# Performance work log

Measured on AMD Instinct MI355X. Metric: run time of the kernel, lower is better.

## Reference

```python
import jax, jax.numpy as jnp
import numpy as np

F_DIM = 64; HID = 256; P_ETA = 32; NBINS = 16; MULT = 3 * NBINS - 1
NLAYERS = 8; NBLOCKS = 2; TAIL = 10.0
MIN_BW = 1e-8; MIN_BH = 1e-8; MIN_D = 1e-8
THETA_DIM = F_DIM + 1
N_BATCH = 8192; M_DATA = 256


def _masks():
    in_deg = np.arange(1, F_DIM + 1)
    hid_deg = np.arange(HID) % (F_DIM - 1) + 1
    out_deg = np.repeat(in_deg, MULT)  # output index f*MULT+m has degree f+1
    m_in = (hid_deg[:, None] >= in_deg[None, :]).astype(np.float32)
    m_hh = (hid_deg[:, None] >= hid_deg[None, :]).astype(np.float32)
    m_out = (out_deg[:, None] > hid_deg[None, :]).astype(np.float32)
    return jnp.asarray(m_in), jnp.asarray(m_hh), jnp.asarray(m_out)


def _rqs_forward(x, uw, uh, ud):
    # unconstrained rational-quadratic spline with linear tails (nflows math)
    const = float(np.log(np.exp(1.0 - MIN_D) - 1.0))
    inside = (x >= -TAIL) & (x <= TAIL)
    ud = jnp.pad(ud, ((0, 0), (0, 0), (1, 1)), constant_values=const)  # [N,F,NBINS+1]
    w = jax.nn.softmax(uw, -1)
    w = MIN_BW + (1.0 - MIN_BW * NBINS) * w
    cw = jnp.concatenate([jnp.zeros_like(w[..., :1]), jnp.cumsum(w, -1)], -1)
    cw = 2.0 * TAIL * cw - TAIL
    cw = cw.at[..., 0].set(-TAIL).at[..., -1].set(TAIL)
    w = jnp.diff(cw, axis=-1)
    h = jax.nn.softmax(uh, -1)
    h = MIN_BH + (1.0 - MIN_BH * NBINS) * h
    ch = jnp.concatenate([jnp.zeros_like(h[..., :1]), jnp.cumsum(h, -1)], -1)
    ch = 2.0 * TAIL * ch - TAIL
    ch = ch.at[..., 0].set(-TAIL).at[..., -1].set(TAIL)
    h = jnp.diff(ch, axis=-1)
    d = MIN_D + jax.nn.softplus(ud)
    xs = jnp.clip(x, -TAIL, TAIL)
    idx = jnp.clip(jnp.sum((xs[..., None] >= cw).astype(jnp.int32), -1) - 1, 0, NBINS - 1)
    g = lambda a, i: jnp.take_along_axis(a, i[..., None], -1)[..., 0]
    icw, ich = g(cw, idx), g(ch, idx)
    iw, ih = g(w, idx), g(h, idx)
    delta = ih / iw
    d0, d1 = g(d, idx), g(d, idx + 1)
    t = (xs - icw) / iw
    tt = t * (1.0 - t)
    denom = delta + (d0 + d1 - 2.0 * delta) * tt
    y = ich + ih * (delta * t * t + d0 * tt) / denom
    dnum = delta * delta * (d1 * t * t + 2.0 * delta * tt + d0 * (1.0 - t) * (1.0 - t))
    ld = jnp.log(dnum) - 2.0 * jnp.log(denom)
    return jnp.where(inside, y, x), jnp.where(inside, ld, 0.0)


def _flow_transform(z, eta, W_in, b_in, W_ctx, b_ctx, W_blk, b_blk, W_out, b_out):
    m_in, m_hh, m_out = _masks()
    sqrt_h = jnp.sqrt(jnp.asarray(HID, z.dtype))

    def layer(carry, p):
        x, ld = carry
        Wi, bi, Wc, bc, Wb, bb, Wo, bo = p
        x = jnp.flip(x, axis=1)  # ReversePermutation (logdet 0)
        h = x @ (Wi * m_in).T + bi + eta @ Wc.T + bc  # MADE initial + context
        for k in range(NBLOCKS):  # masked pre-activation residual blocks
            t = jax.nn.relu(h)
            t = t @ (Wb[k, 0] * m_hh).T + bb[k, 0]
            t = jax.nn.relu(t)
            t = t @ (Wb[k, 1] * m_hh).T + bb[k, 1]
            h = h + t
        out = (h @ (Wo * m_out).T + bo).reshape(x.shape[0], F_DIM, MULT)
        uw = out[..., :NBINS] / sqrt_h
        uh = out[..., NBINS:2 * NBINS] / sqrt_h
        ud = out[..., 2 * NBINS:]
        x, l = _rqs_forward(x, uw, uh, ud)
        return (x, ld + l.sum(-1)), None

    init = (z, jnp.zeros(z.shape[0], z.dtype))
    (x, ld), _ = jax.lax.scan(layer, init, (W_in, b_in, W_ctx, b_ctx, W_blk, b_blk, W_out, b_out))
    return x, ld


def _stick_breaking(x):
    log_v = -jax.nn.softplus(-x)
    log_1v = -jax.nn.softplus(x)
    prefix = jnp.concatenate([jnp.zeros_like(x[:, :1]), jnp.cumsum(log_1v[:, :-1], 1)], 1)
    log_theta = jnp.concatenate([log_v + prefix, log_1v.sum(1, keepdims=True)], 1)
    wts = jnp.arange(F_DIM, 0, -1, dtype=x.dtype)
    log_det = log_v.sum(1) + (wts * log_1v).sum(1)
    return jnp.exp(log_theta), log_det


def setup_inputs() -> dict:
    key = jax.random.key(0)
    ks = jax.random.split(key, 8)
    s = 0.05
    return {
        'z': jax.random.normal(ks[0], (N_BATCH, F_DIM), jnp.float32),
        'eta_batch': jax.random.normal(ks[1], (N_BATCH, P_ETA), jnp.float32),
        'data_D2': jax.random.normal(ks[2], (M_DATA, THETA_DIM), jnp.float32),
        'W_in': s * jax.random.normal(ks[3], (NLAYERS, HID, F_DIM), jnp.float32),
        'b_in': jnp.zeros((NLAYERS, HID), jnp.float32),
        'W_ctx': s * jax.random.normal(ks[4], (NLAYERS, HID, P_ETA), jnp.float32),
        'b_ctx': jnp.zeros((NLAYERS, HID), jnp.float32),
        'W_blk': s * jax.random.normal(ks[5], (NLAYERS, NBLOCKS, 2, HID, HID), jnp.float32),
        'b_blk': jnp.zeros((NLAYERS, NBLOCKS, 2, HID), jnp.float32),
        'W_out': s * jax.random.normal(ks[6], (NLAYERS, F_DIM * MULT, HID), jnp.float32),
        'b_out': jnp.zeros((NLAYERS, F_DIM * MULT), jnp.float32),
    }


def reference(z, eta_batch, data_D2, W_in, b_in, W_ctx, b_ctx, W_blk, b_blk, W_out, b_out):
    x, flow_ld = _flow_transform(z, eta_batch, W_in, b_in, W_ctx, b_ctx, W_blk, b_blk, W_out, b_out)
    theta, sb_ld = _stick_breaking(x)
    total_ld = flow_ld + sb_ld
    log_qz = -0.5 * jnp.sum(z * z, -1) - 0.5 * F_DIM * jnp.log(2.0 * jnp.pi).astype(z.dtype)
    log_q = log_qz - total_ld
    # prior: Dirichlet(alpha=2) unnormalized: sum log(theta)
    log_p = jnp.sum(jnp.log(jnp.clip(theta, 1e-10, None)), -1)
    # likelihood: mean over data rows of isotropic Gaussian centered at theta
    d_sq = jnp.mean(jnp.sum(data_D2 * data_D2, -1))
    d_mean = jnp.mean(data_D2, 0)
    log_lik = -0.5 * (d_sq - 2.0 * theta @ d_mean + jnp.sum(theta * theta, -1))
    return jnp.mean(log_q - (log_p + log_lik))
```

## Files before the change

### kernel.cpp

```cpp
#include <hip/hip_runtime.h>
#include <hip/hip_fp8.h>
#include <math.h>

typedef float f32x4 __attribute__((ext_vector_type(4)));
typedef unsigned short u16;
typedef unsigned char u8;

typedef const __attribute__((address_space(1))) unsigned int ga_u32;
typedef __attribute__((address_space(3))) unsigned int ls_u32;

__device__ __forceinline__ void gl16(const void* g, void* l) {
    __builtin_amdgcn_global_load_lds((ga_u32*)g, (ls_u32*)l, 16, 0, 0);
}

__device__ __forceinline__ u16 f2bf(float f) {
    union { float f; unsigned u; } v; v.f = f;
    return (u16)((v.u + 0x7FFFu + ((v.u >> 16) & 1u)) >> 16);
}
__device__ __forceinline__ float bf2f(u16 h) {
    union { unsigned u; float f; } v; v.u = ((unsigned)h) << 16;
    return v.f;
}
__device__ __forceinline__ u8 f2q(float f) {
    __hip_fp8_e4m3 t(f);
    return (u8)t.__x;
}
__device__ __forceinline__ long ld8(const u8* p) { return *(const long*)p; }

__device__ __forceinline__ float splusf(float x) {
    return fmaxf(x, 0.f) + __logf(1.f + __expf(-fabsf(x)));
}
__device__ __forceinline__ int invperm(int k) {
    int m, q;
    if (k < 20) { m = k / 5; q = k - 5 * m; }
    else        { m = (k - 4) >> 2; q = (k - 4) & 3; }
    return m + 63 * q;
}

#define MID_ACT_P 272
#define WSCALE 64.f
#define WINV (1.f / 64.f)

__global__ __launch_bounds__(256) void setup_w(
    const float* __restrict__ Win, const float* __restrict__ bin,
    const float* __restrict__ Wctx, const float* __restrict__ bctx,
    const float* __restrict__ Wblk, const float* __restrict__ Wout,
    const float* __restrict__ bout, const float* __restrict__ eta,
    u8* __restrict__ W1, float* __restrict__ B1, u8* __restrict__ WB,
    u8* __restrict__ WO, float* __restrict__ BO, u8* __restrict__ AXE)
{
    const long N1 = 8L * 8 * 8 * 64 * 8;
    const long N2 = 8L * 256;
    const long N3 = 8L * 4 * 8 * 16 * 64 * 8;
    const long N4 = 8L * 32 * 8 * 6 * 64 * 8;
    const long N5 = 8L * 3072;
    const long N6 = 8192L * 32;
    const long tot = N1 + N2 + N3 + N4 + N5 + N6;
    for (long i = (long)blockIdx.x * blockDim.x + threadIdx.x; i < tot;
         i += (long)gridDim.x * blockDim.x) {
        long t = i;
        if (t < N1) {
            int off = (int)(t & 7), lane = (int)((t >> 3) & 63);
            int frag = (int)((t >> 9) & 7), wv = (int)((t >> 12) & 7);
            long l = t >> 15;
            int ks = frag >> 1, f = frag & 1;
            int prow = wv * 32 + f * 16 + (lane & 15);
            int row = invperm(prow);
            int c = ks * 32 + ((lane >> 4) << 3) + off;
            float v = 0.f;
            if (c < 64)      v = Win[(l * 256 + row) * 64 + c] * (((row % 63) >= c) ? 1.f : 0.f);
            else if (c < 96) v = Wctx[(l * 256 + row) * 32 + (c - 64)];
            W1[t] = f2q(v * WSCALE);
        } else if ((t -= N1) < N2) {
            long l = t >> 8; int k = (int)(t & 255);
            int c = invperm(k);
            B1[t] = bin[l * 256 + c] + bctx[l * 256 + c];
        } else if ((t -= N2) < N3) {
            int off = (int)(t & 7), lane = (int)((t >> 3) & 63);
            int frag = (int)((t >> 9) & 15), wv = (int)((t >> 13) & 7);
            int bi = (int)((t >> 16) & 3);
            long l = t >> 18;
            int prow = wv * 32 + (frag & 1) * 16 + (lane & 15);
            int pc   = ((frag >> 1) << 5) + ((lane >> 4) << 3) + off;
            int row = invperm(prow), c = invperm(pc);
            float v = Wblk[(((size_t)l * 4 + bi) * 256 + row) * 256 + c] *
                      (((row % 63) >= (c % 63)) ? 1.f : 0.f);
            WB[t] = f2q(v * WSCALE);
        } else if ((t -= N3) < N4) {
            long l = t / 786432; int rem = (int)(t % 786432);
            int y = rem / 24576, r2 = rem % 24576;
            int ks = r2 / 3072, r3 = r2 % 3072;
            int frag = r3 / 512, r4 = r3 % 512;
            int lane = r4 / 8, off = r4 % 8;
            int op = y * 96 + frag * 16 + (lane & 15);
            int pj = ks * 32 + ((lane >> 4) << 3) + off;
            int j = invperm(pj);
            int fd = op / 48, mm = op % 48;
            float v = 0.f;
            if (mm < 47 && fd > (j % 63))
                v = Wout[((size_t)l * 3008 + fd * 47 + mm) * 256 + j];
            WO[t] = f2q(v * WSCALE);
        } else if ((t -= N4) < N5) {
            long l = t / 3072; int op = (int)(t % 3072);
            int fd = op / 48, mm = op % 48;
            BO[t] = (mm < 47) ? bout[l * 3008 + (long)fd * 47 + mm] : 0.f;
        } else {
            t -= N5;
            long b = t / 32; int p = (int)(t % 32);
            AXE[b * 96 + 64 + p] = f2q(eta[t]);
        }
    }
}

__global__ __launch_bounds__(256) void perm_bias(
    const float* __restrict__ bblk, float* __restrict__ BBp)
{
    int t = blockIdx.x * 256 + threadIdx.x;
    int k = t & 255;
    BBp[t] = bblk[(t & ~255) | invperm(k)];
}

__global__ __launch_bounds__(128) void dstat(const float* __restrict__ D,
                                             float* __restrict__ DM)
{
    int j = threadIdx.x;
    float s = 0.f, q = 0.f;
    if (j < 65) {
        for (int m = 0; m < 256; ++m) {
            float v = D[m * 65 + j];
            s += v; q += v * v;
        }
        DM[j] = s * (1.f / 256.f);
    }
    __shared__ float red[128];
    red[j] = q; __syncthreads();
    for (int st = 64; st > 0; st >>= 1) {
        if (j < st) red[j] += red[j + st];
        __syncthreads();
    }
    if (j == 0) DM[65] = red[0] * (1.f / 256.f);
}

__global__ __launch_bounds__(256) void prep0(
    const float* __restrict__ z, float* __restrict__ XF, u8* __restrict__ AXE)
{
    size_t gt = (size_t)blockIdx.x * 256 + threadIdx.x;
    size_t b = gt >> 6; int f = (int)(gt & 63);
    float v = z[b * 64 + (63 - f)];
    XF[gt] = v;
    AXE[b * 96 + f] = f2q(v);
}

template<int NF>
__device__ __forceinline__ void mid_stage_reg(
    const u8* __restrict__ gW, const u8* __restrict__ act,
    int lane, int fr, int kg, f32x4 (&T)[2])
{
    long wf[NF];
#pragma unroll
    for (int j = 0; j < NF; ++j)
        wf[j] = ld8(gW + (j * 64 + lane) * 8);
#pragma unroll
    for (int ks = 0; ks < NF / 2; ++ks) {
        long af = ld8(&act[fr * MID_ACT_P + ks * 32 + kg * 8]);
        T[0] = __builtin_amdgcn_mfma_f32_16x16x32_fp8_fp8(wf[ks * 2 + 0], af, T[0], 0, 0, 0);
        T[1] = __builtin_amdgcn_mfma_f32_16x16x32_fp8_fp8(wf[ks * 2 + 1], af, T[1], 0, 0, 0);
    }
}

__global__ __launch_bounds__(512) void fused_mid(
    const u8* __restrict__ AXE, const u8* __restrict__ W1l,
    const float* __restrict__ B1l, const u8* __restrict__ WBl,
    const float* __restrict__ bbl, u8* __restrict__ HB)
{
    __shared__ u8 act[16 * MID_ACT_P];
    const int tid = threadIdx.x;
    const int lane = tid & 63;
    const int wv = tid >> 6;
    const int fr = lane & 15, kg = lane >> 4;
    const int b0 = blockIdx.x * 16;
    const int ch0 = wv * 32;

    if (tid < 96) {
        int row = tid / 6, part = tid - row * 6;
        *(int4*)&act[row * MID_ACT_P + part * 16] =
            *(const int4*)&AXE[(size_t)(b0 + row) * 96 + part * 16];
    }

    f32x4 H[2], T[2];

    auto zeroT = [&]() {
        T[0] = (f32x4){0.f, 0.f, 0.f, 0.f};
        T[1] = (f32x4){0.f, 0.f, 0.f, 0.f};
    };
    auto epi = [&](const float* bias, int mode) {
#pragma unroll
        for (int m = 0; m < 2; ++m) {
            const int cb = ch0 + m * 16 + kg * 4;
            const float4 bs = *(const float4*)&bias[cb];
            f32x4 v = T[m];
            v[0] = v[0] * WINV + bs.x; v[1] = v[1] * WINV + bs.y;
            v[2] = v[2] * WINV + bs.z; v[3] = v[3] * WINV + bs.w;
            if (mode == 0) H[m] = v;
            if (mode == 2 || mode == 3) {
                H[m][0] += v[0]; H[m][1] += v[1];
                H[m][2] += v[2]; H[m][3] += v[3];
                v = H[m];
            }
            unsigned pk;
            if (mode != 3) {
                pk = (unsigned)f2q(fmaxf(v[0], 0.f))
                   | ((unsigned)f2q(fmaxf(v[1], 0.f)) << 8)
                   | ((unsigned)f2q(fmaxf(v[2], 0.f)) << 16)
                   | ((unsigned)f2q(fmaxf(v[3], 0.f)) << 24);
                *(unsigned*)&act[fr * MID_ACT_P + cb] = pk;
            } else {
                pk = (unsigned)f2q(v[0]) | ((unsigned)f2q(v[1]) << 8)
                   | ((unsigned)f2q(v[2]) << 16) | ((unsigned)f2q(v[3]) << 24);
                const int b = b0 + fr;
                const size_t idx =
                    (((((size_t)(b >> 7) * 8 + (cb >> 5)) * 8 + ((b >> 4) & 7)) * 64)
                     + (((cb >> 3) & 3) * 16 + (b & 15))) * 8 + (cb & 7);
                *(unsigned*)&HB[idx] = pk;
            }
        }
    };

    zeroT();
    __syncthreads();
    mid_stage_reg<6>(W1l + wv * 4096, act, lane, fr, kg, T);
    __syncthreads();
    epi(B1l, 0);
    zeroT();
    __syncthreads();
    mid_stage_reg<16>(WBl + 0 * 65536 + wv * 8192, act, lane, fr, kg, T);
    __syncthreads();
    epi(bbl, 1);
    zeroT();
    __syncthreads();
    mid_stage_reg<16>(WBl + 1 * 65536 + wv * 8192, act, lane, fr, kg, T);
    __syncthreads();
    epi(bbl + 256, 2);
    zeroT();
    __syncthreads();
    mid_stage_reg<16>(WBl + 2 * 65536 + wv * 8192, act, lane, fr, kg, T);
    __syncthreads();
    epi(bbl + 2 * 256, 1);
    zeroT();
    __syncthreads();
    mid_stage_reg<16>(WBl + 3 * 65536 + wv * 8192, act, lane, fr, kg, T);
    __syncthreads();
    epi(bbl + 3 * 256, 3);
}

__global__ __launch_bounds__(256) void gemm_out_spline(
    const u8* __restrict__ A, const u8* __restrict__ Wo,
    const float* __restrict__ bo, const float* __restrict__ XF,
    float* __restrict__ Xn, float* __restrict__ XFnext, u8* __restrict__ AXE,
    float* __restrict__ LDP, int first)
{
    __shared__ u16 SM16[13312];
    u8* SM8 = (u8*)SM16;
    const int tid = threadIdx.x;
    const int lane = tid & 63, wv = tid >> 6;
    const int wm = wv >> 1, wn = wv & 1;
    const int fr = lane & 15, kg = lane >> 4;
    const int by = 31 - (int)blockIdx.y;
    const int m0 = blockIdx.x * 128, n0 = by * 96;
    const int nk = (by + 4) >> 2;

    u8* Ab = SM8;
    u8* Bb = SM8 + 8192;

    const u8* gA = A  + (size_t)blockIdx.x * 16384;
    const u8* gB = Wo + (size_t)by * 24576;

    f32x4 acc[4][3];
#pragma unroll
    for (int m = 0; m < 4; ++m)
#pragma unroll
        for (int n = 0; n < 3; ++n) acc[m][n] = (f32x4){0.f, 0.f, 0.f, 0.f};

    gl16(gA + tid * 16, Ab + tid * 16);
    if (tid < 192) gl16(gB + tid * 16, Bb + tid * 16);

    for (int ks = 0; ks < nk; ++ks) {
        __syncthreads();
        if (ks + 1 < nk) {
            const u8* sa = gA + (ks + 1) * 4096;
            const u8* sb = gB + (ks + 1) * 3072;
            u8* na = Ab + ((ks + 1) & 1) * 4096;
            u8* nb = Bb + ((ks + 1) & 1) * 3072;
            gl16(sa + tid * 16, na + tid * 16);
            if (tid < 192) gl16(sb + tid * 16, nb + tid * 16);
        }
        const u8* cA = Ab + (ks & 1) * 4096;
        const u8* cB = Bb + (ks & 1) * 3072;
        long af[4], bf[3];
#pragma unroll
        for (int m = 0; m < 4; ++m)
            af[m] = ld8(&cA[(wm * 4 + m) * 512 + lane * 8]);
#pragma unroll
        for (int n = 0; n < 3; ++n)
            bf[n] = ld8(&cB[(wn * 3 + n) * 512 + lane * 8]);
#pragma unroll
        for (int m = 0; m < 4; ++m)
#pragma unroll
            for (int n = 0; n < 3; ++n)
                acc[m][n] = __builtin_amdgcn_mfma_f32_16x16x32_fp8_fp8(bf[n], af[m], acc[m][n], 0, 0, 0);
    }
    __syncthreads();

#pragma unroll
    for (int m = 0; m < 4; ++m) {
        const int row = wm * 64 + m * 16 + fr;
#pragma unroll
        for (int n = 0; n < 3; ++n) {
            const int c0 = wn * 48 + n * 16 + kg * 4;
            const float4 bs = *(const float4*)&bo[n0 + c0];
            short4 q;
            q.x = (short)f2bf(acc[m][n][0] * WINV + bs.x);
            q.y = (short)f2bf(acc[m][n][1] * WINV + bs.y);
            q.z = (short)f2bf(acc[m][n][2] * WINV + bs.z);
            q.w = (short)f2bf(acc[m][n][3] * WINV + bs.w);
            *(short4*)&SM16[row * 104 + c0] = q;
        }
    }
    __syncthreads();

    typedef short bf16x8 __attribute__((ext_vector_type(8)));
    const int r = tid >> 1, fi = tid & 1;
    const int b = m0 + r;
    const int fg = by * 2 + fi;
    const u16* o_ = &SM16[r * 104 + fi * 48];
    bf16x8 v0 = *(const bf16x8*)(o_);
    bf16x8 v1 = *(const bf16x8*)(o_ + 8);
    bf16x8 v2 = *(const bf16x8*)(o_ + 16);
    bf16x8 v3 = *(const bf16x8*)(o_ + 24);
    bf16x8 v4 = *(const bf16x8*)(o_ + 32);
    bf16x8 v5 = *(const bf16x8*)(o_ + 40);

    float xin = XF[(size_t)b * 64 + fg];
    bool inside = (xin >= -10.f) && (xin <= 10.f);
    float xs = fminf(fmaxf(xin, -10.f), 10.f);

    float ew[16], eh[16], ud[15];
#pragma unroll
    for (int i = 0; i < 8; ++i) {
        ew[i]     = bf2f((u16)v0[i]) * 0.0625f;
        ew[8 + i] = bf2f((u16)v1[i]) * 0.0625f;
        eh[i]     = bf2f((u16)v2[i]) * 0.0625f;
        eh[8 + i] = bf2f((u16)v3[i]) * 0.0625f;
    }
#pragma unroll
    for (int i = 0; i < 8; ++i) ud[i] = bf2f((u16)v4[i]);
#pragma unroll
    for (int i = 0; i < 7; ++i) ud[8 + i] = bf2f((u16)v5[i]);

    float mw = ew[0], mh = eh[0];
#pragma unroll
    for (int i = 1; i < 16; ++i) { mw = fmaxf(mw, ew[i]); mh = fmaxf(mh, eh[i]); }
    float sw = 0.f, sh = 0.f;
#pragma unroll
    for (int i = 0; i < 16; ++i) {
        ew[i] = __expf(ew[i] - mw); sw += ew[i];
        eh[i] = __expf(eh[i] - mh); sh += eh[i];
    }
    const float kw = 20.f * (1.f - 1.6e-7f) / sw;
    const float kh = 20.f * (1.f - 1.6e-7f) / sh;

    float cwk = -10.f, chk = -10.f;
    float icw = -10.f, ich = -10.f, iw = 1.f, ih = 1.f, udl = 0.f, udr = 0.f;
    int selk = 0;
#pragma unroll
    for (int k = 0; k < 16; ++k) {
        const float cw1 = (k == 15) ? 10.f : cwk + (2e-7f + kw * ew[k]);
        const float ch1 = (k == 15) ? 10.f : chk + (2e-7f + kh * eh[k]);
        if (xs >= cwk) {
            selk = k;
            icw = cwk; iw = cw1 - cwk;
            ich = chk; ih = ch1 - chk;
            udl = (k >= 1)  ? ud[k - 1] : 0.f;
            udr = (k <= 14) ? ud[k]     : 0.f;
        }
        cwk = cw1; chk = ch1;
    }
    float d0 = (selk == 0)  ? 1.f : 1e-8f + splusf(udl);
    float d1 = (selk == 15) ? 1.f : 1e-8f + splusf(udr);
    float delta = ih / iw;
    float t = (xs - icw) / iw;
    float tt = t * (1.f - t);
    float denom = delta + (d0 + d1 - 2.f * delta) * tt;
    float y = ich + ih * (delta * t * t + d0 * tt) / denom;
    float omt = 1.f - t;
    float dnum = delta * delta * (d1 * t * t + 2.f * delta * tt + d0 * omt * omt);
    float ldv = __logf(dnum) - 2.f * __logf(denom);
    if (!inside) { y = xin; ldv = 0.f; }

    Xn[(size_t)b * 64 + fg] = y;
    XFnext[(size_t)b * 64 + (63 - fg)] = y;
    AXE[(size_t)b * 96 + (63 - fg)] = f2q(y);

    float other = __shfl_xor(ldv, 1);
    if (fi == 0) {
        size_t o = (size_t)b * 32 + by;
        float v = ldv + other;
        LDP[o] = first ? v : (LDP[o] + v);
    }
}

__global__ __launch_bounds__(256) void final1(
    const float* __restrict__ X, const float* __restrict__ z,
    const float* __restrict__ LDP, const float* __restrict__ DM,
    float* __restrict__ PART)
{
    int tid = threadIdx.x;
    int b = blockIdx.x * 256 + tid;
    float ldt = 0.f;
    for (int g = 0; g < 32; ++g) ldt += LDP[(size_t)b * 32 + g];
    float pre = 0.f, lvs = 0.f, wls = 0.f, lp = 0.f, tdm = 0.f, tsq = 0.f;
    const float LCLIP = -23.02585093f;
    for (int i = 0; i < 64; ++i) {
        float xi = X[(size_t)b * 64 + i];
        float lv = -splusf(-xi), l1 = -splusf(xi);
        float lt = lv + pre;
        float th = __expf(lt);
        lp += fmaxf(lt, LCLIP);
        tdm += th * DM[i]; tsq += th * th;
        lvs += lv; wls += (float)(64 - i) * l1;
        pre += l1;
    }
    float th = __expf(pre);
    lp += fmaxf(pre, LCLIP); tdm += th * DM[64]; tsq += th * th;
    float zs = 0.f;
    for (int i = 0; i < 64; ++i) { float zz = z[(size_t)b * 64 + i]; zs += zz * zz; }
    float logqz = -0.5f * zs - 58.812066f;
    float log_q = logqz - (ldt + lvs + wls);
    float log_lik = -0.5f * (DM[65] - 2.f * tdm + tsq);
    float val = log_q - lp - log_lik;

    __shared__ float red[256];
    red[tid] = val; __syncthreads();
    for (int s = 128; s > 0; s >>= 1) {
        if (tid < s) red[tid] += red[tid + s];
        __syncthreads();
    }
    if (tid == 0) PART[blockIdx.x] = red[0];
}

__global__ __launch_bounds__(64) void final2(const float* __restrict__ PART,
                                             float* __restrict__ out)
{
    int tid = threadIdx.x;
    float s = (tid < 32) ? PART[tid] : 0.f;
    for (int o = 16; o > 0; o >>= 1) s += __shfl_down(s, o);
    if (tid == 0) out[0] = s * (1.f / 8192.f);
}

extern "C" void kernel_launch(void* const* d_in, const int* in_sizes, int n_in,
                              void* d_out, int out_size, void* d_ws, size_t ws_size,
                              hipStream_t stream)
{
    (void)in_sizes; (void)n_in; (void)out_size; (void)ws_size;
    const float* z    = (const float*)d_in[0];
    const float* eta  = (const float*)d_in[1];
    const float* dat  = (const float*)d_in[2];
    const float* Win  = (const float*)d_in[3];
    const float* bin  = (const float*)d_in[4];
    const float* Wctx = (const float*)d_in[5];
    const float* bctx = (const float*)d_in[6];
    const float* Wblk = (const float*)d_in[7];
    const float* bblk = (const float*)d_in[8];
    const float* Wout = (const float*)d_in[9];
    const float* bout = (const float*)d_in[10];
    float* out = (float*)d_out;

    char* w = (char*)d_ws;
    size_t off = 0;
    auto alloc = [&](size_t bytes) {
        void* p = w + off;
        off += (bytes + 255) & ~(size_t)255;
        return p;
    };
    u8*    W1  = (u8*)   alloc(8L * 32768);
    float* B1  = (float*)alloc(8L * 256 * 4);
    u8*    WB  = (u8*)   alloc(8L * 262144);
    float* BBp = (float*)alloc(8L * 4 * 256 * 4);
    u8*    WO  = (u8*)   alloc(8L * 786432);
    float* BO  = (float*)alloc(8L * 3072 * 4);
    u8*    AXE = (u8*)   alloc(8192L * 96);
    float* XFa = (float*)alloc(8192L * 64 * 4);
    float* XFb = (float*)alloc(8192L * 64 * 4);
    float* XC  = (float*)alloc(8192L * 64 * 4);
    u8*    HB  = (u8*)   alloc(8192L * 256);
    float* LDP = (float*)alloc(8192L * 32 * 4);
    float* DM  = (float*)alloc(66 * 4);
    float* PART= (float*)alloc(64 * 4);

    setup_w<<<dim3(2048), dim3(256), 0, stream>>>(
        Win, bin, Wctx, bctx, Wblk, Wout, bout, eta,
        W1, B1, WB, WO, BO, AXE);
    perm_bias<<<dim3(32), dim3(256), 0, stream>>>(bblk, BBp);
    dstat<<<dim3(1), dim3(128), 0, stream>>>(dat, DM);
    prep0<<<dim3(2048), dim3(256), 0, stream>>>(z, XFa, AXE);

    for (int l = 0; l < 8; ++l) {
        float* XFin  = (l & 1) ? XFb : XFa;
        float* XFout = (l & 1) ? XFa : XFb;
        fused_mid<<<dim3(512), dim3(512), 0, stream>>>(
            AXE, W1 + (size_t)l * 32768, B1 + l * 256,
            WB + (size_t)l * 262144, BBp + (size_t)l * 4 * 256, HB);
        gemm_out_spline<<<dim3(64, 32), dim3(256), 0, stream>>>(
            HB, WO + (size_t)l * 786432, BO + l * 3072, XFin,
            XC, XFout, AXE, LDP, (l == 0) ? 1 : 0);
    }
    final1<<<dim3(32), dim3(256), 0, stream>>>(XC, z, LDP, DM, PART);
    final2<<<dim3(1), dim3(64), 0, stream>>>(PART, out);
}
```

Baseline: 314.6 us.

## Skip zero MADE-masked k-blocks in hidden GEMMs with balanced row-block pairing

The hidden-to-hidden weights are MADE-masked and block-triangular after permutation, so each 16-row output block only needs k-slices up to its diagonal. Each wave now owns row blocks wv and 15-wv, which gives every wave 9 k-fragments instead of 16 and keeps the load balanced. The packed weight buffer shrinks to match, cutting both MFMA work and weight bytes loaded per block. The first-stage weight loads are also issued before the barrier so they overlap the activation staging. Correctness relies on the permutation making the mask exactly block-triangular at 32-wide k granularity.

```diff
diff --git a/kernel.cpp b/kernel.cpp
--- a/kernel.cpp
+++ b/kernel.cpp
@@ -51,7 +51,7 @@
 {
     const long N1 = 8L * 8 * 8 * 64 * 8;
     const long N2 = 8L * 256;
-    const long N3 = 8L * 4 * 8 * 16 * 64 * 8;
+    const long N3 = 8L * 4 * 8 * 9 * 64 * 8;
     const long N4 = 8L * 32 * 8 * 6 * 64 * 8;
     const long N5 = 8L * 3072;
     const long N6 = 8192L * 32;
@@ -64,7 +64,8 @@
             int frag = (int)((t >> 9) & 7), wv = (int)((t >> 12) & 7);
             long l = t >> 15;
             int ks = frag >> 1, f = frag & 1;
-            int prow = wv * 32 + f * 16 + (lane & 15);
+            int pblk = f ? (15 - wv) : wv;
+            int prow = pblk * 16 + (lane & 15);
             int row = invperm(prow);
             int c = ks * 32 + ((lane >> 4) << 3) + off;
             float v = 0.f;
@@ -77,11 +78,17 @@
             B1[t] = bin[l * 256 + c] + bctx[l * 256 + c];
         } else if ((t -= N2) < N3) {
             int off = (int)(t & 7), lane = (int)((t >> 3) & 63);
-            int frag = (int)((t >> 9) & 15), wv = (int)((t >> 13) & 7);
-            int bi = (int)((t >> 16) & 3);
-            long l = t >> 18;
-            int prow = wv * 32 + (frag & 1) * 16 + (lane & 15);
-            int pc   = ((frag >> 1) << 5) + ((lane >> 4) << 3) + off;
+            long r5 = t >> 9;
+            int frag = (int)(r5 % 9); long r6 = r5 / 9;
+            int wv = (int)(r6 & 7);
+            int bi = (int)((r6 >> 3) & 3);
+            long l = r6 >> 5;
+            int kA = (wv + 2) >> 1;
+            int pblk, ksl;
+            if (frag < kA) { pblk = wv;      ksl = frag; }
+            else           { pblk = 15 - wv; ksl = frag - kA; }
+            int prow = pblk * 16 + (lane & 15);
+            int pc   = ksl * 32 + ((lane >> 4) << 3) + off;
             int row = invperm(prow), c = invperm(pc);
             float v = Wblk[(((size_t)l * 4 + bi) * 256 + row) * 256 + c] *
                       (((row % 63) >= (c % 63)) ? 1.f : 0.f);
@@ -151,20 +158,25 @@
     AXE[b * 96 + f] = f2q(v);
 }
 
-template<int NF>
-__device__ __forceinline__ void mid_stage_reg(
+template<int KA>
+__device__ __forceinline__ void wb_stage(
     const u8* __restrict__ gW, const u8* __restrict__ act,
-    int lane, int fr, int kg, f32x4 (&T)[2])
-{
-    long wf[NF];
-#pragma unroll
-    for (int j = 0; j < NF; ++j)
+    int lane, int fr, int kg, f32x4& T0, f32x4& T1)
+{
+    constexpr int KB = 9 - KA;
+    long wf[9];
+#pragma unroll
+    for (int j = 0; j < 9; ++j)
         wf[j] = ld8(gW + (j * 64 + lane) * 8);
 #pragma unroll
-    for (int ks = 0; ks < NF / 2; ++ks) {
-        long af = ld8(&act[fr * MID_ACT_P + ks * 32 + kg * 8]);
-        T[0] = __builtin_amdgcn_mfma_f32_16x16x32_fp8_fp8(wf[ks * 2 + 0], af, T[0], 0, 0, 0);
-        T[1] = __builtin_amdgcn_mfma_f32_16x16x32_fp8_fp8(wf[ks * 2 + 1], af, T[1], 0, 0, 0);
+    for (int j = 0; j < KA; ++j) {
+        long af = ld8(&act[fr * MID_ACT_P + j * 32 + kg * 8]);
+        T0 = __builtin_amdgcn_mfma_f32_16x16x32_fp8_fp8(wf[j], af, T0, 0, 0, 0);
+    }
+#pragma unroll
+    for (int j = 0; j < KB; ++j) {
+        long af = ld8(&act[fr * MID_ACT_P + j * 32 + kg * 8]);
+        T1 = __builtin_amdgcn_mfma_f32_16x16x32_fp8_fp8(wf[KA + j], af, T1, 0, 0, 0);
     }
 }
 
@@ -179,7 +191,8 @@
     const int wv = tid >> 6;
     const int fr = lane & 15, kg = lane >> 4;
     const int b0 = blockIdx.x * 16;
-    const int ch0 = wv * 32;
+    const int cbA = wv * 16 + kg * 4;
+    const int cbB = (15 - wv) * 16 + kg * 4;
 
     if (tid < 96) {
         int row = tid / 6, part = tid - row * 6;
@@ -187,68 +200,87 @@
             *(const int4*)&AXE[(size_t)(b0 + row) * 96 + part * 16];
     }
 
-    f32x4 H[2], T[2];
+    f32x4 H0, H1, T0, T1;
 
     auto zeroT = [&]() {
-        T[0] = (f32x4){0.f, 0.f, 0.f, 0.f};
-        T[1] = (f32x4){0.f, 0.f, 0.f, 0.f};
+        T0 = (f32x4){0.f, 0.f, 0.f, 0.f};
+        T1 = (f32x4){0.f, 0.f, 0.f, 0.f};
+    };
+    auto epi1 = [&](f32x4& T, f32x4& H, int cb, const float* bias, int mode) {
+        const float4 bs = *(const float4*)&bias[cb];
+        f32x4 v = T;
+        v[0] = v[0] * WINV + bs.x; v[1] = v[1] * WINV + bs.y;
+        v[2] = v[2] * WINV + bs.z; v[3] = v[3] * WINV + bs.w;
+        if (mode == 0) H = v;
+        if (mode == 2 || mode == 3) {
+            H[0] += v[0]; H[1] += v[1]; H[2] += v[2]; H[3] += v[3];
+            v = H;
+        }
+        unsigned pk;
+        if (mode != 3) {
+            pk = (unsigned)f2q(fmaxf(v[0], 0.f))
+               | ((unsigned)f2q(fmaxf(v[1], 0.f)) << 8)
+               | ((unsigned)f2q(fmaxf(v[2], 0.f)) << 16)
+               | ((unsigned)f2q(fmaxf(v[3], 0.f)) << 24);
+            *(unsigned*)&act[fr * MID_ACT_P + cb] = pk;
+        } else {
+            pk = (unsigned)f2q(v[0]) | ((unsigned)f2q(v[1]) << 8)
+               | ((unsigned)f2q(v[2]) << 16) | ((unsigned)f2q(v[3]) << 24);
+            const int b = b0 + fr;
+            const size_t idx =
+                (((((size_t)(b >> 7) * 8 + (cb >> 5)) * 8 + ((b >> 4) & 7)) * 64)
+                 + (((cb >> 3) & 3) * 16 + (b & 15))) * 8 + (cb & 7);
+            *(unsigned*)&HB[idx] = pk;
+        }
     };
     auto epi = [&](const float* bias, int mode) {
-#pragma unroll
-        for (int m = 0; m < 2; ++m) {
-            const int cb = ch0 + m * 16 + kg * 4;
-            const float4 bs = *(const float4*)&bias[cb];
-            f32x4 v = T[m];
-            v[0] = v[0] * WINV + bs.x; v[1] = v[1] * WINV + bs.y;
-            v[2] = v[2] * WINV + bs.z; v[3] = v[3] * WINV + bs.w;
-            if (mode == 0) H[m] = v;
-            if (mode == 2 || mode == 3) {
-                H[m][0] += v[0]; H[m][1] += v[1];
-                H[m][2] += v[2]; H[m][3] += v[3];
-                v = H[m];
-            }
-            unsigned pk;
-            if (mode != 3) {
-                pk = (unsigned)f2q(fmaxf(v[0], 0.f))
-                   | ((unsigned)f2q(fmaxf(v[1], 0.f)) << 8)
-                   | ((unsigned)f2q(fmaxf(v[2], 0.f)) << 16)
-                   | ((unsigned)f2q(fmaxf(v[3], 0.f)) << 24);
-                *(unsigned*)&act[fr * MID_ACT_P + cb] = pk;
-            } else {
-                pk = (unsigned)f2q(v[0]) | ((unsigned)f2q(v[1]) << 8)
-                   | ((unsigned)f2q(v[2]) << 16) | ((unsigned)f2q(v[3]) << 24);
-                const int b = b0 + fr;
-                const size_t idx =
-                    (((((size_t)(b >> 7) * 8 + (cb >> 5)) * 8 + ((b >> 4) & 7)) * 64)
-                     + (((cb >> 3) & 3) * 16 + (b & 15))) * 8 + (cb & 7);
-                *(unsigned*)&HB[idx] = pk;
-            }
-        }
+        epi1(T0, H0, cbA, bias, mode);
+        epi1(T1, H1, cbB, bias, mode);
     };
+    auto wbrun = [&](const u8* gW) {
+        switch (wv >> 1) {
+        case 0: wb_stage<1>(gW, act, lane, fr, kg, T0, T1); break;
+        case 1: wb_stage<2>(gW, act, lane, fr, kg, T0, T1); break;
+        case 2: wb_stage<3>(gW, act, lane, fr, kg, T0, T1); break;
+        default: wb_stage<4>(gW, act, lane, fr, kg, T0, T1); break;
+        }
+    };
 
     zeroT();
-    __syncthreads();
-    mid_stage_reg<6>(W1l + wv * 4096, act, lane, fr, kg, T);
+    {
+        const u8* gW = W1l + wv * 4096;
+        long wf[6];
+#pragma unroll
+        for (int j = 0; j < 6; ++j)
+            wf[j] = ld8(gW + (j * 64 + lane) * 8);
+        __syncthreads();
+#pragma unroll
+        for (int ks = 0; ks < 3; ++ks) {
+            long af = ld8(&act[fr * MID_ACT_P + ks * 32 + kg * 8]);
+            T0 = __builtin_amdgcn_mfma_f32_16x16x32_fp8_fp8(wf[ks * 2 + 0], af, T0, 0, 0, 0);
+            T1 = __builtin_amdgcn_mfma_f32_16x16x32_fp8_fp8(wf[ks * 2 + 1], af, T1, 0, 0, 0);
+        }
+    }
     __syncthreads();
     epi(B1l, 0);
     zeroT();
     __syncthreads();
-    mid_stage_reg<16>(WBl + 0 * 65536 + wv * 8192, act, lane, fr, kg, T);
+    wbrun(WBl + 0 * 36864 + wv * 4608);
     __syncthreads();
     epi(bbl, 1);
     zeroT();
     __syncthreads();
-    mid_stage_reg<16>(WBl + 1 * 65536 + wv * 8192, act, lane, fr, kg, T);
+    wbrun(WBl + 1 * 36864 + wv * 4608);
     __syncthreads();
     epi(bbl + 256, 2);
     zeroT();
     __syncthreads();
-    mid_stage_reg<16>(WBl + 2 * 65536 + wv * 8192, act, lane, fr, kg, T);
+    wbrun(WBl + 2 * 36864 + wv * 4608);
     __syncthreads();
     epi(bbl + 2 * 256, 1);
     zeroT();
     __syncthreads();
-    mid_stage_reg<16>(WBl + 3 * 65536 + wv * 8192, act, lane, fr, kg, T);
+    wbrun(WBl + 3 * 36864 + wv * 4608);
     __syncthreads();
     epi(bbl + 3 * 256, 3);
 }
@@ -484,7 +516,7 @@
     };
     u8*    W1  = (u8*)   alloc(8L * 32768);
     float* B1  = (float*)alloc(8L * 256 * 4);
-    u8*    WB  = (u8*)   alloc(8L * 262144);
+    u8*    WB  = (u8*)   alloc(8L * 147456);
     float* BBp = (float*)alloc(8L * 4 * 256 * 4);
     u8*    WO  = (u8*)   alloc(8L * 786432);
     float* BO  = (float*)alloc(8L * 3072 * 4);
@@ -509,7 +541,7 @@
         float* XFout = (l & 1) ? XFa : XFb;
         fused_mid<<<dim3(512), dim3(512), 0, stream>>>(
             AXE, W1 + (size_t)l * 32768, B1 + l * 256,
-            WB + (size_t)l * 262144, BBp + (size_t)l * 4 * 256, HB);
+            WB + (size_t)l * 147456, BBp + (size_t)l * 4 * 256, HB);
         gemm_out_spline<<<dim3(64, 32), dim3(256), 0, stream>>>(
             HB, WO + (size_t)l * 786432, BO + l * 3072, XFin,
             XC, XFout, AXE, LDP, (l == 0) ? 1 : 0);
```

Measured after the change: 286.1 us. -9.1%, faster.
